# Kernel tuning notes

Measured on AMD Instinct MI355X. Metric: run time of the kernel, lower is better.

The kernel has to match this reference:

```python
import jax, jax.numpy as jnp
import numpy as np

D_MODEL = 1024
NUM_HEADS = 16
HEAD_DIM = D_MODEL // NUM_HEADS
DILATION = 2
SEGMENT = 1024
OFFSET = 0  # head_idx % dilation_rate; head_idx derived from a random param in torch, fixed to 0 here


def setup_inputs() -> dict:
    key = jax.random.key(0)
    x = jax.random.normal(key, (4, 8192, D_MODEL), dtype=jnp.float32)
    return {"x": x}


def reference(x):
    b, n, d = x.shape  # n is already a multiple of SEGMENT (no padding needed)
    n_seg = n // SEGMENT
    k = SEGMENT // DILATION  # sparse tokens kept per segment

    # dilated gather: within each segment keep every DILATION-th token
    local_idx = OFFSET + DILATION * jnp.arange(k)                      # [k]
    global_idx = SEGMENT * jnp.arange(n_seg)[:, None] + local_idx[None, :]  # [n_seg, k]
    xs = x[:, global_idx, :]                                           # [b, n_seg, k, d]

    # multi-head self-attention within each sparse segment (q = k = v = xs)
    qh = xs.reshape(b, n_seg, k, NUM_HEADS, HEAD_DIM)
    scale = 1.0 / jnp.sqrt(jnp.asarray(HEAD_DIM, dtype=xs.dtype))
    scores = jnp.einsum('bsqhd,bskhd->bshqk', qh, qh) * scale          # [b, n_seg, h, k, k]
    attn = jax.nn.softmax(scores, axis=-1)
    seg_out = jnp.einsum('bshqk,bskhd->bsqhd', attn, qh)
    a_os = seg_out.reshape(b, n_seg * k, d)                            # [b, M, d]

    # mix_outputs: denominator-weighted scatter-add merge back to full sequence
    idx = jnp.broadcast_to(global_idx.reshape(-1), (b, n_seg * k))     # [b, M] global positions
    a_denoms = a_os.sum(axis=-1)                                       # [b, M]

    def mix(o_b, den_b, idx_b):
        sums = jnp.zeros((n,), o_b.dtype).at[idx_b].add(den_b)         # scatter_add of denoms
        alphas = den_b / sums[idx_b]                                   # gather + divide
        return jnp.zeros((n, d), o_b.dtype).at[idx_b].add(o_b * alphas[:, None])

    return jax.vmap(mix)(a_os, a_denoms, idx)                          # [b, n, d]
```

## Files before the change

kernel.cpp:

```cpp
#include <hip/hip_runtime.h>
#include <math.h>

#define NSEQ 8192
#define DM 1024
#define DH 64
#define SEG 1024
#define CH 128
#define NCH 4
#define KTS 72
#define VTS 136
#define PS  136

typedef __attribute__((ext_vector_type(8))) short short8;
typedef __attribute__((ext_vector_type(4))) float floatx4;

__device__ __forceinline__ unsigned pk_bf16x2(float a, float b) {
  unsigned x = __float_as_uint(a), y = __float_as_uint(b);
  x += 0x7fffu + ((x >> 16) & 1u);
  y += 0x7fffu + ((y >> 16) & 1u);
  return (x >> 16) | (y & 0xffff0000u);
}

__global__ __launch_bounds__(256, 4)
void dilattn_kernel(const float* __restrict__ x, float* __restrict__ out) {
  __shared__ unsigned short Kt[CH * KTS];
  __shared__ unsigned short VT[DH * VTS];

  const int i = blockIdx.x;
  const int bs = (i & 7) | ((i >> 10) << 3);
  const int hq = (i >> 3) & 127;
  const int b = bs >> 3, s = bs & 7;
  const int h = hq >> 3, qt = hq & 7;
  const float* xb = x + ((size_t)b * NSEQ + (size_t)s * SEG) * DM;
  float* outb = out + ((size_t)b * NSEQ + (size_t)s * SEG) * DM;
  const int tid = threadIdx.x;
  const int lane = tid & 63;
  const int w = tid >> 6;
  const int cq = lane & 15;
  const int u = lane >> 4;
  const int q0 = qt * 64 + w * 16;

  {
    const float4 z = make_float4(0.f, 0.f, 0.f, 0.f);
    #pragma unroll
    for (int it = 0; it < 4; ++it) {
      int idx = tid + 256 * it;
      int j = idx >> 4, c4 = idx & 15;
      *(float4*)(outb + (size_t)(2 * (qt * 64 + j) + 1) * DM + h * DH + c4 * 4) = z;
    }
  }

  short8 qf[2];
  {
    const float* xq = xb + (size_t)(2 * (q0 + cq)) * DM + h * DH;
    #pragma unroll
    for (int ks = 0; ks < 2; ++ks) {
      float4 a = *(const float4*)(xq + 32 * ks + 8 * u);
      float4 c = *(const float4*)(xq + 32 * ks + 8 * u + 4);
      union { unsigned u4[4]; short8 s8; } pk;
      pk.u4[0] = pk_bf16x2(a.x, a.y);
      pk.u4[1] = pk_bf16x2(a.z, a.w);
      pk.u4[2] = pk_bf16x2(c.x, c.y);
      pk.u4[3] = pk_bf16x2(c.z, c.w);
      qf[ks] = pk.s8;
    }
  }

  floatx4 o[4];
  #pragma unroll
  for (int nt = 0; nt < 4; ++nt) o[nt] = (floatx4){0.f, 0.f, 0.f, 0.f};
  float l = 0.f;
  const float cf = 0.125f * 1.44269504088896340736f;

  const int c8 = tid & 7;
  const int sr = tid >> 3;
  const int vd = tid & 63;
  const int vg = tid >> 6;

  for (int c = 0; c < NCH; ++c) {
    #pragma unroll
    for (int pass = 0; pass < 4; ++pass) {
      int r = pass * 32 + sr;
      const float* src = xb + (size_t)(2 * (c * CH + r)) * DM + h * DH + c8 * 8;
      float4 a = *(const float4*)(src);
      float4 d2 = *(const float4*)(src + 4);
      union { unsigned u4[4]; short8 s8; } pk;
      pk.u4[0] = pk_bf16x2(a.x, a.y);
      pk.u4[1] = pk_bf16x2(a.z, a.w);
      pk.u4[2] = pk_bf16x2(d2.x, d2.y);
      pk.u4[3] = pk_bf16x2(d2.z, d2.w);
      *(short8*)(Kt + r * KTS + c8 * 8) = pk.s8;
    }
    #pragma unroll
    for (int g8 = 0; g8 < 4; ++g8) {
      float v[8];
      #pragma unroll
      for (int j = 0; j < 8; ++j)
        v[j] = xb[(size_t)(2 * (c * CH + vg * 32 + g8 * 8 + j)) * DM + h * DH + vd];
      union { unsigned u4[4]; short8 s8; } pk;
      #pragma unroll
      for (int m = 0; m < 4; ++m) pk.u4[m] = pk_bf16x2(v[2 * m], v[2 * m + 1]);
      *(short8*)(VT + vd * VTS + vg * 32 + g8 * 8) = pk.s8;
    }
    __syncthreads();

    floatx4 st[8];
    #pragma unroll
    for (int t = 0; t < 8; ++t) {
      floatx4 acc = {0.f, 0.f, 0.f, 0.f};
      #pragma unroll
      for (int ks = 0; ks < 2; ++ks) {
        short8 af = *(short8*)(Kt + (t * 16 + cq) * KTS + 32 * ks + 8 * u);
        acc = __builtin_amdgcn_mfma_f32_16x16x32_bf16(af, qf[ks], acc, 0, 0, 0);
      }
      st[t] = acc;
    }
    #pragma unroll
    for (int t = 0; t < 8; ++t)
      #pragma unroll
      for (int r = 0; r < 4; ++r) {
        float p = __builtin_amdgcn_exp2f(st[t][r] * cf);
        st[t][r] = p;
        l += p;
      }
    __syncthreads();

    unsigned short* Pw = Kt + w * 16 * PS;
    #pragma unroll
    for (int t = 0; t < 8; ++t) {
      uint2 pk2;
      pk2.x = pk_bf16x2(st[t][0], st[t][1]);
      pk2.y = pk_bf16x2(st[t][2], st[t][3]);
      *(uint2*)(Pw + cq * PS + t * 16 + 4 * u) = pk2;
    }
    #pragma unroll
    for (int ks = 0; ks < 4; ++ks) {
      short8 pf = *(short8*)(Pw + cq * PS + 32 * ks + 8 * u);
      #pragma unroll
      for (int nt = 0; nt < 4; ++nt) {
        short8 vf = *(short8*)(VT + (nt * 16 + cq) * VTS + 32 * ks + 8 * u);
        o[nt] = __builtin_amdgcn_mfma_f32_16x16x32_bf16(pf, vf, o[nt], 0, 0, 0);
      }
    }
    __syncthreads();
  }

  l += __shfl_xor(l, 16, 64);
  l += __shfl_xor(l, 32, 64);
  float linv[4];
  #pragma unroll
  for (int r = 0; r < 4; ++r) linv[r] = 1.f / __shfl(l, 4 * u + r, 64);

  #pragma unroll
  for (int r = 0; r < 4; ++r) {
    float* orow = outb + (size_t)(2 * (q0 + 4 * u + r)) * DM + h * DH + cq;
    #pragma unroll
    for (int nt = 0; nt < 4; ++nt)
      orow[nt * 16] = o[nt][r] * linv[r];
  }
}

extern "C" void kernel_launch(void* const* d_in, const int* in_sizes, int n_in,
                              void* d_out, int out_size, void* d_ws, size_t ws_size,
                              hipStream_t stream) {
  const float* x = (const float*)d_in[0];
  float* out = (float*)d_out;
  dilattn_kernel<<<dim3(4096), dim3(256), 0, stream>>>(x, out);
}
```

Measured before the change: 271.1 us.

## Split into bf16 K/V-transpose prep kernel and async-LDS attention kernel

Adds a prep kernel that converts the dilated tokens once to bf16 in a swizzled K layout and a transposed V layout in workspace, and also zero-fills the odd rows. The attention kernel then uses 512-thread blocks with two query sub-tiles per wave, loads K/V chunks with global_load_lds, and uses swizzled LDS indexing in place of padding. Before, each of the 8 query-tile blocks per head reread and reconverted the fp32 K/V. The change adds a second launch and a workspace round-trip, and falls back to the old kernel when the workspace is too small.

```diff
diff --git a/kernel.cpp b/kernel.cpp
--- a/kernel.cpp
+++ b/kernel.cpp
@@ -1,18 +1,199 @@
 #include <hip/hip_runtime.h>
 #include <math.h>
 
+#define DM 1024
 #define NSEQ 8192
-#define DM 1024
-#define DH 64
-#define SEG 1024
+
+typedef __attribute__((ext_vector_type(8))) short short8;
+typedef __attribute__((ext_vector_type(4))) float floatx4;
+
+__device__ __forceinline__ unsigned pk_rn(float a, float b) {
+  return __builtin_amdgcn_perm(__float_as_uint(b) + 0x8000u,
+                               __float_as_uint(a) + 0x8000u, 0x07060302u);
+}
+
+__device__ __forceinline__ void gload16(const uint4* g, uint4* l) {
+  __builtin_amdgcn_global_load_lds((const __attribute__((address_space(1))) void*)g,
+                                   (__attribute__((address_space(3))) void*)l, 16, 0, 0);
+}
+
+__global__ __launch_bounds__(256, 4)
+void prep_kernel(const float* __restrict__ x, uint4* __restrict__ kbf,
+                 uint4* __restrict__ vt, float* __restrict__ out) {
+  __shared__ uint4 T[1024];
+  const int bid = blockIdx.x;
+  const int tau = bid >> 2, c = bid & 3;
+  const int b = tau >> 7, s = (tau >> 4) & 7, h = tau & 15;
+  const float* xb = x + ((size_t)b * NSEQ + s * 1024) * DM + h * 64;
+  float* ob = out + ((size_t)b * NSEQ + s * 1024) * DM + h * 64;
+  const int tid = threadIdx.x;
+  const int c8 = tid & 7, rr = tid >> 3;
+
+  const float4 z = make_float4(0.f, 0.f, 0.f, 0.f);
+  #pragma unroll
+  for (int p = 0; p < 4; ++p) {
+    int r = p * 32 + rr;
+    int g = c * 128 + r;
+    const float* src = xb + (size_t)(2 * g) * DM + c8 * 8;
+    float4 A = *(const float4*)src;
+    float4 B = *(const float4*)(src + 4);
+    uint4 pk;
+    pk.x = pk_rn(A.x, A.y); pk.y = pk_rn(A.z, A.w);
+    pk.z = pk_rn(B.x, B.y); pk.w = pk_rn(B.z, B.w);
+    T[r * 8 + (c8 ^ (r & 7))] = pk;
+    float* zp = ob + (size_t)(2 * g + 1) * DM + c8 * 8;
+    *(float4*)zp = z;
+    *(float4*)(zp + 4) = z;
+  }
+  __syncthreads();
+
+  uint4* kdst = kbf + (size_t)tau * 4096 + c * 1024;
+  #pragma unroll
+  for (int p = 0; p < 4; ++p) {
+    int L = p * 256 + tid;
+    kdst[L] = T[L];
+  }
+  const unsigned short* Ts = (const unsigned short*)T;
+  uint4* vdst = vt + (size_t)tau * 4096 + c * 1024;
+  #pragma unroll
+  for (int p = 0; p < 4; ++p) {
+    int M = p * 256 + tid;
+    int u16 = M >> 6, dp = M & 63;
+    int d = dp ^ (u16 & 7);
+    unsigned v[8];
+    #pragma unroll
+    for (int j = 0; j < 8; ++j) {
+      int kk = 8 * u16 + j;
+      v[j] = Ts[(kk * 8 + ((d >> 3) ^ (kk & 7))) * 8 + (d & 7)];
+    }
+    uint4 pk;
+    pk.x = v[0] | (v[1] << 16);
+    pk.y = v[2] | (v[3] << 16);
+    pk.z = v[4] | (v[5] << 16);
+    pk.w = v[6] | (v[7] << 16);
+    vdst[M] = pk;
+  }
+}
+
+__global__ __launch_bounds__(512, 4)
+void attn_kernel(const uint4* __restrict__ kbf, const uint4* __restrict__ vt,
+                 float* __restrict__ out) {
+  __shared__ uint4 smem[3072];
+  const int bid = blockIdx.x;
+  const int bs = (bid & 7) | ((bid >> 8) << 3);
+  const int inner = (bid >> 3) & 31;
+  const int h = inner >> 1, qh = inner & 1;
+  const int b = bs >> 3, s = bs & 7;
+  const int tau = bs * 16 + h;
+  const uint4* KT = kbf + (size_t)tau * 4096;
+  const uint4* VTg = vt + (size_t)tau * 4096;
+  float* ob = out + ((size_t)b * NSEQ + s * 1024) * DM + h * 64;
+  const int tid = threadIdx.x;
+  const int lane = tid & 63;
+  const int wu = __builtin_amdgcn_readfirstlane(tid >> 6);
+  const int cq = lane & 15, u = lane >> 4;
+  const int qw0 = qh * 256 + wu * 32;
+
+  short8 qf[2][2];
+  #pragma unroll
+  for (int qs = 0; qs < 2; ++qs) {
+    int R = qw0 + qs * 16 + cq;
+    #pragma unroll
+    for (int ksd = 0; ksd < 2; ++ksd)
+      qf[qs][ksd] = *(const short8*)&KT[(size_t)R * 8 + ((4 * ksd + u) ^ (cq & 7))];
+  }
+
+  floatx4 o[2][4];
+  #pragma unroll
+  for (int qs = 0; qs < 2; ++qs)
+    #pragma unroll
+    for (int nt = 0; nt < 4; ++nt) o[qs][nt] = (floatx4){0.f, 0.f, 0.f, 0.f};
+  float l[2] = {0.f, 0.f};
+  const float cf = 0.125f * 1.44269504088896340736f;
+
+  unsigned short* Pw = (unsigned short*)&smem[2048 + wu * 128];
+  const int pswz = u ^ (cq & 3);
+
+  for (int c = 0; c < 4; ++c) {
+    {
+      const uint4* kg = KT + c * 1024 + wu * 128 + lane;
+      const uint4* vg = VTg + c * 1024 + wu * 128 + lane;
+      gload16(kg, &smem[wu * 128]);
+      gload16(kg + 64, &smem[wu * 128 + 64]);
+      gload16(vg, &smem[1024 + wu * 128]);
+      gload16(vg + 64, &smem[1024 + wu * 128 + 64]);
+    }
+    __syncthreads();
+
+    #pragma unroll
+    for (int ks = 0; ks < 4; ++ks) {
+      floatx4 acc[2][2];
+      #pragma unroll
+      for (int qs = 0; qs < 2; ++qs)
+        #pragma unroll
+        for (int t = 0; t < 2; ++t) acc[qs][t] = (floatx4){0.f, 0.f, 0.f, 0.f};
+      #pragma unroll
+      for (int t = 0; t < 2; ++t) {
+        int r = 16 * (2 * ks + t) + cq;
+        #pragma unroll
+        for (int ksd = 0; ksd < 2; ++ksd) {
+          short8 af = *(short8*)&smem[r * 8 + ((4 * ksd + u) ^ (cq & 7))];
+          #pragma unroll
+          for (int qs = 0; qs < 2; ++qs)
+            acc[qs][t] = __builtin_amdgcn_mfma_f32_16x16x32_bf16(af, qf[qs][ksd], acc[qs][t], 0, 0, 0);
+        }
+      }
+      #pragma unroll
+      for (int qs = 0; qs < 2; ++qs)
+        #pragma unroll
+        for (int t = 0; t < 2; ++t) {
+          float p0 = __builtin_amdgcn_exp2f(acc[qs][t][0] * cf);
+          float p1 = __builtin_amdgcn_exp2f(acc[qs][t][1] * cf);
+          float p2 = __builtin_amdgcn_exp2f(acc[qs][t][2] * cf);
+          float p3 = __builtin_amdgcn_exp2f(acc[qs][t][3] * cf);
+          l[qs] += (p0 + p1) + (p2 + p3);
+          uint2 w2;
+          w2.x = pk_rn(p0, p1);
+          w2.y = pk_rn(p2, p3);
+          int unit = (qs * 16 + cq) * 4 + ((2 * t + (u >> 1)) ^ (cq & 3));
+          *(uint2*)(Pw + unit * 8 + (u & 1) * 4) = w2;
+        }
+      const int u16 = 4 * ks + u;
+      short8 vfr[4];
+      #pragma unroll
+      for (int nt = 0; nt < 4; ++nt)
+        vfr[nt] = *(short8*)&smem[1024 + u16 * 64 + 16 * nt + (cq ^ (u16 & 7))];
+      #pragma unroll
+      for (int qs = 0; qs < 2; ++qs) {
+        short8 pf = *(short8*)(Pw + ((qs * 16 + cq) * 4 + pswz) * 8);
+        #pragma unroll
+        for (int nt = 0; nt < 4; ++nt)
+          o[qs][nt] = __builtin_amdgcn_mfma_f32_16x16x32_bf16(pf, vfr[nt], o[qs][nt], 0, 0, 0);
+      }
+    }
+    __syncthreads();
+  }
+
+  #pragma unroll
+  for (int qs = 0; qs < 2; ++qs) {
+    float lf = l[qs];
+    lf += __shfl_xor(lf, 16, 64);
+    lf += __shfl_xor(lf, 32, 64);
+    #pragma unroll
+    for (int r = 0; r < 4; ++r) {
+      float linv = 1.f / __shfl(lf, 4 * u + r, 64);
+      float* orow = ob + (size_t)(2 * (qw0 + qs * 16 + 4 * u + r)) * DM + cq;
+      #pragma unroll
+      for (int nt = 0; nt < 4; ++nt)
+        orow[nt * 16] = o[qs][nt][r] * linv;
+    }
+  }
+}
+
 #define CH 128
-#define NCH 4
 #define KTS 72
 #define VTS 136
 #define PS  136
-
-typedef __attribute__((ext_vector_type(8))) short short8;
-typedef __attribute__((ext_vector_type(4))) float floatx4;
 
 __device__ __forceinline__ unsigned pk_bf16x2(float a, float b) {
   unsigned x = __float_as_uint(a), y = __float_as_uint(b);
@@ -22,37 +203,34 @@
 }
 
 __global__ __launch_bounds__(256, 4)
-void dilattn_kernel(const float* __restrict__ x, float* __restrict__ out) {
+void dilattn_fallback(const float* __restrict__ x, float* __restrict__ out) {
   __shared__ unsigned short Kt[CH * KTS];
-  __shared__ unsigned short VT[DH * VTS];
-
+  __shared__ unsigned short VT[64 * VTS];
   const int i = blockIdx.x;
   const int bs = (i & 7) | ((i >> 10) << 3);
   const int hq = (i >> 3) & 127;
   const int b = bs >> 3, s = bs & 7;
   const int h = hq >> 3, qt = hq & 7;
-  const float* xb = x + ((size_t)b * NSEQ + (size_t)s * SEG) * DM;
-  float* outb = out + ((size_t)b * NSEQ + (size_t)s * SEG) * DM;
+  const float* xb = x + ((size_t)b * NSEQ + (size_t)s * 1024) * DM;
+  float* outb = out + ((size_t)b * NSEQ + (size_t)s * 1024) * DM;
   const int tid = threadIdx.x;
   const int lane = tid & 63;
   const int w = tid >> 6;
   const int cq = lane & 15;
   const int u = lane >> 4;
   const int q0 = qt * 64 + w * 16;
-
   {
     const float4 z = make_float4(0.f, 0.f, 0.f, 0.f);
     #pragma unroll
     for (int it = 0; it < 4; ++it) {
       int idx = tid + 256 * it;
       int j = idx >> 4, c4 = idx & 15;
-      *(float4*)(outb + (size_t)(2 * (qt * 64 + j) + 1) * DM + h * DH + c4 * 4) = z;
-    }
-  }
-
+      *(float4*)(outb + (size_t)(2 * (qt * 64 + j) + 1) * DM + h * 64 + c4 * 4) = z;
+    }
+  }
   short8 qf[2];
   {
-    const float* xq = xb + (size_t)(2 * (q0 + cq)) * DM + h * DH;
+    const float* xq = xb + (size_t)(2 * (q0 + cq)) * DM + h * 64;
     #pragma unroll
     for (int ks = 0; ks < 2; ++ks) {
       float4 a = *(const float4*)(xq + 32 * ks + 8 * u);
@@ -65,23 +243,20 @@
       qf[ks] = pk.s8;
     }
   }
-
   floatx4 o[4];
   #pragma unroll
   for (int nt = 0; nt < 4; ++nt) o[nt] = (floatx4){0.f, 0.f, 0.f, 0.f};
   float l = 0.f;
   const float cf = 0.125f * 1.44269504088896340736f;
-
   const int c8 = tid & 7;
   const int sr = tid >> 3;
   const int vd = tid & 63;
   const int vg = tid >> 6;
-
-  for (int c = 0; c < NCH; ++c) {
+  for (int c = 0; c < 4; ++c) {
     #pragma unroll
     for (int pass = 0; pass < 4; ++pass) {
       int r = pass * 32 + sr;
-      const float* src = xb + (size_t)(2 * (c * CH + r)) * DM + h * DH + c8 * 8;
+      const float* src = xb + (size_t)(2 * (c * CH + r)) * DM + h * 64 + c8 * 8;
       float4 a = *(const float4*)(src);
       float4 d2 = *(const float4*)(src + 4);
       union { unsigned u4[4]; short8 s8; } pk;
@@ -96,14 +271,13 @@
       float v[8];
       #pragma unroll
       for (int j = 0; j < 8; ++j)
-        v[j] = xb[(size_t)(2 * (c * CH + vg * 32 + g8 * 8 + j)) * DM + h * DH + vd];
+        v[j] = xb[(size_t)(2 * (c * CH + vg * 32 + g8 * 8 + j)) * DM + h * 64 + vd];
       union { unsigned u4[4]; short8 s8; } pk;
       #pragma unroll
       for (int m = 0; m < 4; ++m) pk.u4[m] = pk_bf16x2(v[2 * m], v[2 * m + 1]);
       *(short8*)(VT + vd * VTS + vg * 32 + g8 * 8) = pk.s8;
     }
     __syncthreads();
-
     floatx4 st[8];
     #pragma unroll
     for (int t = 0; t < 8; ++t) {
@@ -124,7 +298,6 @@
         l += p;
       }
     __syncthreads();
-
     unsigned short* Pw = Kt + w * 16 * PS;
     #pragma unroll
     for (int t = 0; t < 8; ++t) {
@@ -144,16 +317,14 @@
     }
     __syncthreads();
   }
-
   l += __shfl_xor(l, 16, 64);
   l += __shfl_xor(l, 32, 64);
   float linv[4];
   #pragma unroll
   for (int r = 0; r < 4; ++r) linv[r] = 1.f / __shfl(l, 4 * u + r, 64);
-
   #pragma unroll
   for (int r = 0; r < 4; ++r) {
-    float* orow = outb + (size_t)(2 * (q0 + 4 * u + r)) * DM + h * DH + cq;
+    float* orow = outb + (size_t)(2 * (q0 + 4 * u + r)) * DM + h * 64 + cq;
     #pragma unroll
     for (int nt = 0; nt < 4; ++nt)
       orow[nt * 16] = o[nt][r] * linv[r];
@@ -165,5 +336,12 @@
                               hipStream_t stream) {
   const float* x = (const float*)d_in[0];
   float* out = (float*)d_out;
-  dilattn_kernel<<<dim3(4096), dim3(256), 0, stream>>>(x, out);
-}
+  if (ws_size >= (size_t)67108864) {
+    uint4* kbf = (uint4*)d_ws;
+    uint4* vt = kbf + (size_t)512 * 4096;
+    prep_kernel<<<dim3(2048), dim3(256), 0, stream>>>(x, kbf, vt, out);
+    attn_kernel<<<dim3(1024), dim3(512), 0, stream>>>(kbf, vt, out);
+  } else {
+    dilattn_fallback<<<dim3(4096), dim3(256), 0, stream>>>(x, out);
+  }
+}
```

New measurement: 265.0 us. 2.2% less time.
